# Kernel tuning notes

Measured on AMD Instinct MI355X. Metric: run time of the kernel, lower is better.

## Reference

```python
import jax, jax.numpy as jnp
import numpy as np

V = 1_000_000  # number of videos
N = 100_000    # batch of query nodes
K = 16         # fixed neighbor degree
D = 128        # emb_dim


def setup_inputs() -> dict:
    key = jax.random.key(0)
    k1, k2, k3, k4, k5 = jax.random.split(key, 5)
    return {
        "video_nodes": jax.random.randint(k1, (N,), 0, V, dtype=jnp.int32),
        "neighbors": jax.random.randint(k2, (N, K), 0, V, dtype=jnp.int32),
        "neigh_weights": jax.random.uniform(k3, (N, K), dtype=jnp.float32),
        "video_embeddings": jax.random.normal(k4, (V, D), dtype=jnp.float32),
        "W1": jax.random.normal(k5, (2 * D, D), dtype=jnp.float32) * (1.0 / np.sqrt(2 * D)),
        "b1": jnp.zeros((D,), dtype=jnp.float32),
    }


def reference(video_nodes, neighbors, neigh_weights, video_embeddings, W1, b1):
    # Weighted-mean neighbor aggregation (GraphSAGE-style aggregator).
    w = neigh_weights / jnp.sum(neigh_weights, axis=1, keepdims=True)  # [N,K]
    neigh_emb = video_embeddings[neighbors]                             # [N,K,D]
    neigh_feats = jnp.einsum("nk,nkd->nd", w, neigh_emb)               # [N,D]
    # Self-feature gather.
    self_feats = video_embeddings[video_nodes]                          # [N,D]
    # Concat -> Linear(2D -> D) -> ReLU.
    combined = jnp.concatenate([self_feats, neigh_feats], axis=1)       # [N,2D]
    return jax.nn.relu(combined @ W1 + b1)                              # [N,D]
```

## Files before the change

kernel.cpp:

```cpp
#include <hip/hip_runtime.h>
#include <hip/hip_bf16.h>


#define NN 100000
#define KK 16
#define DD 128
#define MM 16
#define WPB 4

typedef __attribute__((ext_vector_type(8))) short short8;
typedef __attribute__((ext_vector_type(4))) float f32x4;

__global__ __launch_bounds__(256)
void prep_w1t_kernel(const float* __restrict__ W1, __hip_bfloat16* __restrict__ W1T)
{
    const int tid = blockIdx.x * blockDim.x + threadIdx.x;
    const int d = tid >> 8;
    const int k = tid & 255;
    W1T[d * 256 + k] = __float2bfloat16(W1[k * DD + d]);
}

static __device__ __forceinline__ unsigned pk_bf16(float a, float b) {
    __hip_bfloat162 t;
    t.x = __float2bfloat16(a);
    t.y = __float2bfloat16(b);
    return *reinterpret_cast<unsigned*>(&t);
}

__global__ __launch_bounds__(256, 4)
void graphsage_kernel(const int* __restrict__ video_nodes,
                      const int* __restrict__ neighbors,
                      const float* __restrict__ neigh_weights,
                      const float* __restrict__ emb,
                      const __hip_bfloat16* __restrict__ W1T,
                      const float* __restrict__ b1,
                      float* __restrict__ out)
{
    __shared__ __hip_bfloat16 comb[WPB][MM][2 * DD];

    const int lane = threadIdx.x & 63;
    const int wib  = __builtin_amdgcn_readfirstlane(threadIdx.x >> 6);
    const int node0 = (blockIdx.x * WPB + wib) * MM;
    if (node0 >= NN) return;

    char* const slot = (char*)&comb[wib][0][0];
    const char* const embB = (const char*)emb;

    const int half = lane >> 5;
    const int c    = lane & 31;
    const unsigned byte_c = 16u * (unsigned)c;

    #pragma unroll 2
    for (int mp = 0; mp < MM / 2; ++mp) {
        const int n0 = node0 + 2 * mp;
        const int n1 = n0 + 1;

        const int s0i = video_nodes[n0];
        const int s1i = video_nodes[n1];
        const int sidx = half ? s1i : s0i;
        const float4 sv = *reinterpret_cast<const float4*>(
            embB + ((((unsigned)sidx) << 9) + byte_c));

        f32x4 acc = {0.0f, 0.0f, 0.0f, 0.0f};
        float wsum = 0.0f;
        #pragma unroll
        for (int k = 0; k < KK; ++k) {
            const int   i0 = neighbors[n0 * KK + k];
            const int   i1 = neighbors[n1 * KK + k];
            const float w0 = neigh_weights[n0 * KK + k];
            const float w1 = neigh_weights[n1 * KK + k];
            const int   rk = half ? i1 : i0;
            const float wk = half ? w1 : w0;
            wsum += wk;
            const float4 e = *reinterpret_cast<const float4*>(
                embB + ((((unsigned)rk) << 9) + byte_c));
            acc[0] = fmaf(wk, e.x, acc[0]);
            acc[1] = fmaf(wk, e.y, acc[1]);
            acc[2] = fmaf(wk, e.z, acc[2]);
            acc[3] = fmaf(wk, e.w, acc[3]);
        }
        const float inv = 1.0f / wsum;

        const int nodel = 2 * mp + half;
        const unsigned swz = (unsigned)((nodel & 7) << 4);
        const unsigned sb = ((unsigned)(nodel * 512) + 8u * c) ^ swz;
        const unsigned nb = ((unsigned)(nodel * 512 + 256) + 8u * c) ^ swz;

        uint2 sU, nU;
        sU.x = pk_bf16(sv.x, sv.y);
        sU.y = pk_bf16(sv.z, sv.w);
        nU.x = pk_bf16(acc[0] * inv, acc[1] * inv);
        nU.y = pk_bf16(acc[2] * inv, acc[3] * inv);
        *reinterpret_cast<uint2*>(slot + sb) = sU;
        *reinterpret_cast<uint2*>(slot + nb) = nU;
    }

    const int nodeB  = lane & 15;
    const int kchunk = lane >> 4;
    const unsigned swzB = (unsigned)((nodeB & 7) << 4);

    short8 bfrag[8];
    #pragma unroll
    for (int kt = 0; kt < 8; ++kt) {
        const unsigned byte =
            ((unsigned)(nodeB * 512 + kt * 64 + kchunk * 16)) ^ swzB;
        bfrag[kt] = *reinterpret_cast<const short8*>(slot + byte);
    }

    const int drow = lane & 15;
    #pragma unroll
    for (int dt = 0; dt < 8; ++dt) {
        const int d = dt * 16 + drow;
        f32x4 acc = {0.0f, 0.0f, 0.0f, 0.0f};
        #pragma unroll
        for (int kt = 0; kt < 8; ++kt) {
            const short8 afrag = *reinterpret_cast<const short8*>(
                &W1T[d * 256 + kt * 32 + kchunk * 8]);
            acc = __builtin_amdgcn_mfma_f32_16x16x32_bf16(afrag, bfrag[kt], acc,
                                                          0, 0, 0);
        }
        const int node = node0 + (lane & 15);
        const int d0   = dt * 16 + kchunk * 4;
        const float4 bias = *reinterpret_cast<const float4*>(&b1[d0]);
        float4 r;
        r.x = fmaxf(acc[0] + bias.x, 0.0f);
        r.y = fmaxf(acc[1] + bias.y, 0.0f);
        r.z = fmaxf(acc[2] + bias.z, 0.0f);
        r.w = fmaxf(acc[3] + bias.w, 0.0f);
        *reinterpret_cast<float4*>(&out[(size_t)node * DD + d0]) = r;
    }
}

extern "C" void kernel_launch(void* const* d_in, const int* in_sizes, int n_in,
                              void* d_out, int out_size, void* d_ws, size_t ws_size,
                              hipStream_t stream) {
    const int*   video_nodes   = (const int*)d_in[0];
    const int*   neighbors     = (const int*)d_in[1];
    const float* neigh_weights = (const float*)d_in[2];
    const float* emb           = (const float*)d_in[3];
    const float* W1            = (const float*)d_in[4];
    const float* b1            = (const float*)d_in[5];
    float*       out           = (float*)d_out;

    __hip_bfloat16* W1T = (__hip_bfloat16*)d_ws;

    prep_w1t_kernel<<<DD * 256 / 256, 256, 0, stream>>>(W1, W1T);

    const int nodes_per_block = WPB * MM;
    const int grid = (NN + nodes_per_block - 1) / nodes_per_block;
    graphsage_kernel<<<grid, 256, 0, stream>>>(
        video_nodes, neighbors, neigh_weights, emb, W1T, b1, out);
}
```

Baseline: 169.0 us.

## Switch to persistent waves with atomic work-stealing over 32-node chunks

Replaces the one-tile-per-wave grid with a fixed 1024-block persistent grid. Each wave repeatedly grabs 32-node chunks through a global atomic counter, which the prep kernel resets, and processes each chunk as two 16-node tiles. The goal is to balance load across CUs and avoid tail effects and block launch overhead for the latency-bound gather. In exchange it adds atomic contention and a serial dependency per grab, and it relies on NN being divisible by 32.

After: 429.9 us. +154.4%, slower.

```diff
diff --git a/kernel.cpp b/kernel.cpp
--- a/kernel.cpp
+++ b/kernel.cpp
@@ -7,14 +7,18 @@
 #define DD 128
 #define MM 16
 #define WPB 4
+#define GRAB 32
+#define NGRABS (NN / GRAB)
 
 typedef __attribute__((ext_vector_type(8))) short short8;
 typedef __attribute__((ext_vector_type(4))) float f32x4;
 
 __global__ __launch_bounds__(256)
-void prep_w1t_kernel(const float* __restrict__ W1, __hip_bfloat16* __restrict__ W1T)
+void prep_w1t_kernel(const float* __restrict__ W1, __hip_bfloat16* __restrict__ W1T,
+                     int* __restrict__ counter)
 {
     const int tid = blockIdx.x * blockDim.x + threadIdx.x;
+    if (tid == 0) *counter = 0;
     const int d = tid >> 8;
     const int k = tid & 255;
     W1T[d * 256 + k] = __float2bfloat16(W1[k * DD + d]);
@@ -34,14 +38,13 @@
                       const float* __restrict__ emb,
                       const __hip_bfloat16* __restrict__ W1T,
                       const float* __restrict__ b1,
-                      float* __restrict__ out)
+                      float* __restrict__ out,
+                      int* __restrict__ counter)
 {
     __shared__ __hip_bfloat16 comb[WPB][MM][2 * DD];
 
     const int lane = threadIdx.x & 63;
     const int wib  = __builtin_amdgcn_readfirstlane(threadIdx.x >> 6);
-    const int node0 = (blockIdx.x * WPB + wib) * MM;
-    if (node0 >= NN) return;
 
     char* const slot = (char*)&comb[wib][0][0];
     const char* const embB = (const char*)emb;
@@ -50,84 +53,96 @@
     const int c    = lane & 31;
     const unsigned byte_c = 16u * (unsigned)c;
 
-    #pragma unroll 2
-    for (int mp = 0; mp < MM / 2; ++mp) {
-        const int n0 = node0 + 2 * mp;
-        const int n1 = n0 + 1;
+    for (;;) {
+        int grab = 0;
+        if (lane == 0) grab = atomicAdd(counter, 1);
+        grab = __shfl(grab, 0);
+        if (grab >= NGRABS) break;
 
-        const int s0i = video_nodes[n0];
-        const int s1i = video_nodes[n1];
-        const int sidx = half ? s1i : s0i;
-        const float4 sv = *reinterpret_cast<const float4*>(
-            embB + ((((unsigned)sidx) << 9) + byte_c));
+        int node0 = grab * GRAB;
+        #pragma unroll 1
+        for (int t16 = 0; t16 < GRAB / MM; ++t16, node0 += MM) {
 
-        f32x4 acc = {0.0f, 0.0f, 0.0f, 0.0f};
-        float wsum = 0.0f;
-        #pragma unroll
-        for (int k = 0; k < KK; ++k) {
-            const int   i0 = neighbors[n0 * KK + k];
-            const int   i1 = neighbors[n1 * KK + k];
-            const float w0 = neigh_weights[n0 * KK + k];
-            const float w1 = neigh_weights[n1 * KK + k];
-            const int   rk = half ? i1 : i0;
-            const float wk = half ? w1 : w0;
-            wsum += wk;
-            const float4 e = *reinterpret_cast<const float4*>(
-                embB + ((((unsigned)rk) << 9) + byte_c));
-            acc[0] = fmaf(wk, e.x, acc[0]);
-            acc[1] = fmaf(wk, e.y, acc[1]);
-            acc[2] = fmaf(wk, e.z, acc[2]);
-            acc[3] = fmaf(wk, e.w, acc[3]);
+            #pragma unroll 2
+            for (int mp = 0; mp < MM / 2; ++mp) {
+                const int n0 = node0 + 2 * mp;
+                const int n1 = n0 + 1;
+
+                const int s0i = video_nodes[n0];
+                const int s1i = video_nodes[n1];
+                const int sidx = half ? s1i : s0i;
+                const float4 sv = *reinterpret_cast<const float4*>(
+                    embB + ((((unsigned)sidx) << 9) + byte_c));
+
+                f32x4 acc = {0.0f, 0.0f, 0.0f, 0.0f};
+                float wsum = 0.0f;
+                #pragma unroll
+                for (int k = 0; k < KK; ++k) {
+                    const int   i0 = neighbors[n0 * KK + k];
+                    const int   i1 = neighbors[n1 * KK + k];
+                    const float w0 = neigh_weights[n0 * KK + k];
+                    const float w1 = neigh_weights[n1 * KK + k];
+                    const int   rk = half ? i1 : i0;
+                    const float wk = half ? w1 : w0;
+                    wsum += wk;
+                    const float4 e = *reinterpret_cast<const float4*>(
+                        embB + ((((unsigned)rk) << 9) + byte_c));
+                    acc[0] = fmaf(wk, e.x, acc[0]);
+                    acc[1] = fmaf(wk, e.y, acc[1]);
+                    acc[2] = fmaf(wk, e.z, acc[2]);
+                    acc[3] = fmaf(wk, e.w, acc[3]);
+                }
+                const float inv = 1.0f / wsum;
+
+                const int nodel = 2 * mp + half;
+                const unsigned swz = (unsigned)((nodel & 7) << 4);
+                const unsigned sb = ((unsigned)(nodel * 512) + 8u * c) ^ swz;
+                const unsigned nb = ((unsigned)(nodel * 512 + 256) + 8u * c) ^ swz;
+
+                uint2 sU, nU;
+                sU.x = pk_bf16(sv.x, sv.y);
+                sU.y = pk_bf16(sv.z, sv.w);
+                nU.x = pk_bf16(acc[0] * inv, acc[1] * inv);
+                nU.y = pk_bf16(acc[2] * inv, acc[3] * inv);
+                *reinterpret_cast<uint2*>(slot + sb) = sU;
+                *reinterpret_cast<uint2*>(slot + nb) = nU;
+            }
+
+            const int nodeB  = lane & 15;
+            const int kchunk = lane >> 4;
+            const unsigned swzB = (unsigned)((nodeB & 7) << 4);
+
+            short8 bfrag[8];
+            #pragma unroll
+            for (int kt = 0; kt < 8; ++kt) {
+                const unsigned byte =
+                    ((unsigned)(nodeB * 512 + kt * 64 + kchunk * 16)) ^ swzB;
+                bfrag[kt] = *reinterpret_cast<const short8*>(slot + byte);
+            }
+
+            const int drow = lane & 15;
+            #pragma unroll
+            for (int dt = 0; dt < 8; ++dt) {
+                const int d = dt * 16 + drow;
+                f32x4 acc = {0.0f, 0.0f, 0.0f, 0.0f};
+                #pragma unroll
+                for (int kt = 0; kt < 8; ++kt) {
+                    const short8 afrag = *reinterpret_cast<const short8*>(
+                        &W1T[d * 256 + kt * 32 + kchunk * 8]);
+                    acc = __builtin_amdgcn_mfma_f32_16x16x32_bf16(
+                        afrag, bfrag[kt], acc, 0, 0, 0);
+                }
+                const int node = node0 + (lane & 15);
+                const int d0   = dt * 16 + kchunk * 4;
+                const float4 bias = *reinterpret_cast<const float4*>(&b1[d0]);
+                float4 r;
+                r.x = fmaxf(acc[0] + bias.x, 0.0f);
+                r.y = fmaxf(acc[1] + bias.y, 0.0f);
+                r.z = fmaxf(acc[2] + bias.z, 0.0f);
+                r.w = fmaxf(acc[3] + bias.w, 0.0f);
+                *reinterpret_cast<float4*>(&out[(size_t)node * DD + d0]) = r;
+            }
         }
-        const float inv = 1.0f / wsum;
-
-        const int nodel = 2 * mp + half;
-        const unsigned swz = (unsigned)((nodel & 7) << 4);
-        const unsigned sb = ((unsigned)(nodel * 512) + 8u * c) ^ swz;
-        const unsigned nb = ((unsigned)(nodel * 512 + 256) + 8u * c) ^ swz;
-
-        uint2 sU, nU;
-        sU.x = pk_bf16(sv.x, sv.y);
-        sU.y = pk_bf16(sv.z, sv.w);
-        nU.x = pk_bf16(acc[0] * inv, acc[1] * inv);
-        nU.y = pk_bf16(acc[2] * inv, acc[3] * inv);
-        *reinterpret_cast<uint2*>(slot + sb) = sU;
-        *reinterpret_cast<uint2*>(slot + nb) = nU;
-    }
-
-    const int nodeB  = lane & 15;
-    const int kchunk = lane >> 4;
-    const unsigned swzB = (unsigned)((nodeB & 7) << 4);
-
-    short8 bfrag[8];
-    #pragma unroll
-    for (int kt = 0; kt < 8; ++kt) {
-        const unsigned byte =
-            ((unsigned)(nodeB * 512 + kt * 64 + kchunk * 16)) ^ swzB;
-        bfrag[kt] = *reinterpret_cast<const short8*>(slot + byte);
-    }
-
-    const int drow = lane & 15;
-    #pragma unroll
-    for (int dt = 0; dt < 8; ++dt) {
-        const int d = dt * 16 + drow;
-        f32x4 acc = {0.0f, 0.0f, 0.0f, 0.0f};
-        #pragma unroll
-        for (int kt = 0; kt < 8; ++kt) {
-            const short8 afrag = *reinterpret_cast<const short8*>(
-                &W1T[d * 256 + kt * 32 + kchunk * 8]);
-            acc = __builtin_amdgcn_mfma_f32_16x16x32_bf16(afrag, bfrag[kt], acc,
-                                                          0, 0, 0);
-        }
-        const int node = node0 + (lane & 15);
-        const int d0   = dt * 16 + kchunk * 4;
-        const float4 bias = *reinterpret_cast<const float4*>(&b1[d0]);
-        float4 r;
-        r.x = fmaxf(acc[0] + bias.x, 0.0f);
-        r.y = fmaxf(acc[1] + bias.y, 0.0f);
-        r.z = fmaxf(acc[2] + bias.z, 0.0f);
-        r.w = fmaxf(acc[3] + bias.w, 0.0f);
-        *reinterpret_cast<float4*>(&out[(size_t)node * DD + d0]) = r;
     }
 }
 
@@ -143,11 +158,11 @@
     float*       out           = (float*)d_out;
 
     __hip_bfloat16* W1T = (__hip_bfloat16*)d_ws;
+    int* counter = (int*)((char*)d_ws + (128 * 256 * 2));
 
-    prep_w1t_kernel<<<DD * 256 / 256, 256, 0, stream>>>(W1, W1T);
+    prep_w1t_kernel<<<DD * 256 / 256, 256, 0, stream>>>(W1, W1T, counter);
 
-    const int nodes_per_block = WPB * MM;
-    const int grid = (NN + nodes_per_block - 1) / nodes_per_block;
+    const int grid = 1024;
     graphsage_kernel<<<grid, 256, 0, stream>>>(
-        video_nodes, neighbors, neigh_weights, emb, W1T, b1, out);
+        video_nodes, neighbors, neigh_weights, emb, W1T, b1, out, counter);
 }
```
